# Performance work log

Hardware: AMD Instinct MI355X
Metric: run time of the kernel (lower is better)

## Reference

```python
import jax, jax.numpy as jnp
import numpy as np

N = 100000   # nodes
E = 1600000  # edges (avg degree 16)
R = 8        # relations
B = 4        # bases
IN = 128     # in_size
H = 128      # hidden_size
OUT = 64     # out_feats


def setup_inputs() -> dict:
    key = jax.random.key(0)
    k = jax.random.split(key, 14)
    sI = 1.0 / np.sqrt(IN)
    sH = 1.0 / np.sqrt(H)
    sB = 1.0 / np.sqrt(B)
    return {
        "feat": jax.random.normal(k[0], (N, IN), jnp.float32),
        "win": jax.random.normal(k[1], (IN, H), jnp.float32) * sI,
        "bin_": jnp.zeros((H,), jnp.float32),
        "basis0": jax.random.normal(k[2], (B, H, H), jnp.float32) * sH,
        "wcomp0": jax.random.normal(k[3], (R, B), jnp.float32) * sB,
        "loop0": jax.random.normal(k[4], (H, H), jnp.float32) * sH,
        "hbias0": jnp.zeros((H,), jnp.float32),
        "basis1": jax.random.normal(k[5], (B, H, H), jnp.float32) * sH,
        "wcomp1": jax.random.normal(k[6], (R, B), jnp.float32) * sB,
        "loop1": jax.random.normal(k[7], (H, H), jnp.float32) * sH,
        "hbias1": jnp.zeros((H,), jnp.float32),
        "wout": jax.random.normal(k[8], (H, OUT), jnp.float32) * sH,
        "bout": jnp.zeros((OUT,), jnp.float32),
        "src": jax.random.randint(k[9], (E,), 0, N),
        "dst": jax.random.randint(k[10], (E,), 0, N),
        "etypes": jax.random.randint(k[11], (E,), 0, R),
    }


def _rel_graph_conv(h, src, dst, etypes, basis, wcomp, loopw, hbias):
    """DGL RelGraphConv (basis regularizer, self_loop, bias, relu).

    out_i = relu( sum_r W_r * (sum_{e: dst_e=i, etype_e=r} h[src_e]) + h_i @ loopw + bias )
    Messages are linear, so we aggregate raw features by (dst, relation)
    composite key first, then apply the R per-relation matmuls once per node.
    """
    W = jnp.einsum('rb,bio->rio', wcomp, basis)          # [R, H, H] basis-composed weights
    seg = dst * R + etypes                               # composite (node, relation) key
    s = jax.ops.segment_sum(h[src], seg, num_segments=N * R)  # [N*R, H]
    s = s.reshape(N, R, -1)
    agg = jnp.einsum('nri,rio->no', s, W)                # [N, H]
    return jax.nn.relu(agg + hbias + h @ loopw)


def reference(feat, win, bin_, basis0, wcomp0, loop0, hbias0,
              basis1, wcomp1, loop1, hbias1, wout, bout, src, dst, etypes):
    h = jax.nn.relu(feat @ win + bin_)                   # input_layer
    h = _rel_graph_conv(h, src, dst, etypes, basis0, wcomp0, loop0, hbias0)
    h = _rel_graph_conv(h, src, dst, etypes, basis1, wcomp1, loop1, hbias1)
    return jax.nn.relu(h @ wout + bout)                  # out_layer
```

## Files before the change

kernel.cpp:

```cpp
#include <hip/hip_runtime.h>

#define NN   100000
#define EE   1600000
constexpr int RR = 8;
constexpr int BBASES = 4;
constexpr int SCAN_CHUNK = 1024;
constexpr int NBLK = (NN + SCAN_CHUNK - 1) / SCAN_CHUNK;
constexpr int NBUK = 98;
constexpr int EPB  = 4096;
constexpr int P1BLOCKS = (EE + EPB - 1) / EPB;

typedef __attribute__((ext_vector_type(8))) short short8;
typedef __attribute__((ext_vector_type(4))) float f32x4;

__device__ __forceinline__ unsigned pack2(float x, float y) {
    unsigned xu = __float_as_uint(x);
    unsigned yu = __float_as_uint(y);
    xu = (xu + 0x7fffu + ((xu >> 16) & 1u)) >> 16;
    yu = (yu + 0x7fffu + ((yu >> 16) & 1u)) & 0xffff0000u;
    return xu | yu;
}

__device__ __forceinline__ unsigned short bf16r(float x) {
    unsigned u = __float_as_uint(x);
    return (unsigned short)((u + 0x7fffu + ((u >> 16) & 1u)) >> 16);
}

__device__ __forceinline__ void async16(const void* g, void* l) {
    __builtin_amdgcn_global_load_lds(
        (const __attribute__((address_space(1))) void*)g,
        (__attribute__((address_space(3))) void*)l, 16, 0, 0);
}


__global__ __launch_bounds__(256) void count_kernel(const int* __restrict__ dst,
                                                    int* __restrict__ counts) {
    int e = blockIdx.x * 256 + threadIdx.x;
    if (e < EE) atomicAdd(&counts[dst[e]], 1);
}

__global__ __launch_bounds__(256) void scan1(const int* __restrict__ counts,
                                             int* __restrict__ offsets,
                                             int* __restrict__ totals) {
    __shared__ int lds[256];
    int b = blockIdx.x, tid = threadIdx.x;
    int base = b * SCAN_CHUNK + tid * 4;
    int v0 = (base + 0 < NN) ? counts[base + 0] : 0;
    int v1 = (base + 1 < NN) ? counts[base + 1] : 0;
    int v2 = (base + 2 < NN) ? counts[base + 2] : 0;
    int v3 = (base + 3 < NN) ? counts[base + 3] : 0;
    int s0 = v0, s1 = s0 + v1, s2 = s1 + v2, s3 = s2 + v3;
    lds[tid] = s3;
    __syncthreads();
    for (int d = 1; d < 256; d <<= 1) {
        int x = (tid >= d) ? lds[tid - d] : 0;
        __syncthreads();
        lds[tid] += x;
        __syncthreads();
    }
    int incl = lds[tid];
    int prefix = incl - s3;
    if (base + 0 < NN) offsets[base + 0] = prefix;
    if (base + 1 < NN) offsets[base + 1] = prefix + s0;
    if (base + 2 < NN) offsets[base + 2] = prefix + s1;
    if (base + 3 < NN) offsets[base + 3] = prefix + s2;
    if (tid == 255) totals[b] = lds[255];
}

__global__ __launch_bounds__(128) void scan2(int* __restrict__ totals,
                                             int* __restrict__ offsets,
                                             int* __restrict__ gcursor) {
    __shared__ int s[128];
    int tid = threadIdx.x;
    int v = (tid < NBLK) ? totals[tid] : 0;
    s[tid] = v;
    __syncthreads();
    for (int d = 1; d < 128; d <<= 1) {
        int x = (tid >= d) ? s[tid - d] : 0;
        __syncthreads();
        s[tid] += x;
        __syncthreads();
    }
    int excl = s[tid] - v;
    if (tid < NBLK) {
        totals[tid] = excl;
        gcursor[tid] = excl;
    }
    if (tid == NBLK - 1) offsets[NN] = excl + v;
}

__global__ __launch_bounds__(256) void scan3(int* __restrict__ offsets,
                                             const int* __restrict__ totals) {
    int i = blockIdx.x * 256 + threadIdx.x;
    if (i < NN) offsets[i] += totals[i >> 10];
}


__global__ __launch_bounds__(256) void bin_pass1(const int* __restrict__ src,
                                                 const int* __restrict__ dst,
                                                 const int* __restrict__ et,
                                                 int* __restrict__ gcursor,
                                                 unsigned* __restrict__ tmp) {
    __shared__ unsigned stage[EPB];
    __shared__ int hist[128];
    __shared__ int sc[128];
    __shared__ int lb[128];
    __shared__ int gb[128];
    int tid = threadIdx.x;
    long e0 = (long)blockIdx.x * EPB;
    if (tid < 128) hist[tid] = 0;
    __syncthreads();

    unsigned w[16];
    int bk[16], pos[16];
#pragma unroll
    for (int i = 0; i < 16; ++i) {
        long e = e0 + i * 256 + tid;
        bool valid = e < EE;
        int d = valid ? dst[e] : 0;
        int s = valid ? src[e] : 0;
        int r = valid ? et[e] : 0;
        bk[i] = d >> 10;
        w[i] = (unsigned)s | ((unsigned)r << 17) | ((unsigned)(d & 1023) << 20);
        pos[i] = valid ? atomicAdd(&hist[bk[i]], 1) : -1;
    }
    __syncthreads();
    if (tid < 128) sc[tid] = hist[tid];
    __syncthreads();
    for (int d = 1; d < 128; d <<= 1) {
        int v = 0;
        if (tid < 128 && tid >= d) v = sc[tid - d];
        __syncthreads();
        if (tid < 128) sc[tid] += v;
        __syncthreads();
    }
    if (tid < 128) lb[tid] = sc[tid] - hist[tid];
    if (tid < NBUK && hist[tid] > 0) gb[tid] = atomicAdd(&gcursor[tid], hist[tid]);
    __syncthreads();
    int total = sc[127];
#pragma unroll
    for (int i = 0; i < 16; ++i) {
        if (pos[i] >= 0) stage[lb[bk[i]] + pos[i]] = w[i];
    }
    __syncthreads();
    for (int s = tid; s < total; s += 256) {
        int lo = 0, hi = 127;
#pragma unroll
        for (int it = 0; it < 7; ++it) {
            int mid = (lo + hi + 1) >> 1;
            if (lb[mid] <= s) lo = mid; else hi = mid - 1;
        }
        tmp[gb[lo] + (s - lb[lo])] = stage[s];
    }
}

__global__ __launch_bounds__(1024) void bin_pass2(const unsigned* __restrict__ tmp,
                                                  const int* __restrict__ offsets,
                                                  int* __restrict__ packed) {
    __shared__ int cur[1024];
    __shared__ int offs[1025];
    int b = blockIdx.x, tid = threadIdx.x;
    int nb0 = b << 10;
    int nend = nb0 + 1024; if (nend > NN) nend = NN;
    int nloc = nend - nb0;
    cur[tid] = 0;
    for (int i = tid; i <= nloc; i += 1024) offs[i] = offsets[nb0 + i];
    __syncthreads();
    int beg = offs[0], end = offs[nloc];
    for (int e = beg + tid; e < end; e += 1024) {
        unsigned wv = tmp[e];
        int dl = (wv >> 20) & 1023;
        int p = offs[dl] + atomicAdd(&cur[dl], 1);
        packed[p] = (int)((wv & 0x1FFFFu) | (((wv >> 17) & 7u) << 20));
    }
}


__global__ __launch_bounds__(256) void convert_weights(const float* __restrict__ basis0,
                                                       const float* __restrict__ loop0,
                                                       const float* __restrict__ basis1,
                                                       const float* __restrict__ loop1,
                                                       const float* __restrict__ win,
                                                       const float* __restrict__ wout,
                                                       unsigned short* __restrict__ BT0,
                                                       unsigned short* __restrict__ BT1,
                                                       unsigned short* __restrict__ winT,
                                                       unsigned short* __restrict__ woutT) {
    int i = blockIdx.x * 256 + threadIdx.x;
    if (i < 81920) {
        int n = i / 640, k = i % 640;
        BT0[i] = bf16r(k < 512 ? basis0[(size_t)k * 128 + n] : loop0[(size_t)(k - 512) * 128 + n]);
    } else if (i < 163840) {
        int j = i - 81920;
        int n = j / 640, k = j % 640;
        BT1[j] = bf16r(k < 512 ? basis1[(size_t)k * 128 + n] : loop1[(size_t)(k - 512) * 128 + n]);
    } else if (i < 180224) {
        int j = i - 163840;
        int n = j >> 7, k = j & 127;
        winT[j] = bf16r(win[(size_t)k * 128 + n]);
    } else if (i < 188416) {
        int j = i - 180224;
        int n = j >> 7, k = j & 127;
        woutT[j] = bf16r(wout[(size_t)k * 64 + n]);
    }
}

template <int NC, bool F32OUT, bool AF32>
__global__ __launch_bounds__(256) void gemm128(const void* __restrict__ Aptr,
                                               const unsigned short* __restrict__ BT,
                                               const float* __restrict__ bias,
                                               void* __restrict__ outp, int M) {
    constexpr int NFRAG = NC / 32;
    constexpr int BQ = NC * 8 / 256;
    __shared__ __align__(16) char As[2][16384];
    __shared__ __align__(16) char Bs[2][NC * 128];
    int tid = threadIdx.x;
    int lane = tid & 63;
    int wave = tid >> 6;
    int wm = wave >> 1, wn = wave & 1;
    int m0 = blockIdx.x * 128;

    uint4 areg[4], breg[BQ];
    auto loadA = [&](int c) {
#pragma unroll
        for (int q = 0; q < 4; ++q) {
            int lin = q * 256 + tid;
            int row = lin >> 3, slot = lin & 7;
            int gr = m0 + row;
            gr = (gr < M) ? gr : (M - 1);
            if (AF32) {
                const float* fp = (const float*)Aptr + (size_t)gr * 128 + c * 64 + slot * 8;
                float4 v0 = *(const float4*)fp;
                float4 v1 = *(const float4*)(fp + 4);
                areg[q].x = pack2(v0.x, v0.y);
                areg[q].y = pack2(v0.z, v0.w);
                areg[q].z = pack2(v1.x, v1.y);
                areg[q].w = pack2(v1.z, v1.w);
            } else {
                areg[q] = *(const uint4*)((const char*)Aptr + (size_t)gr * 256 + c * 128 + slot * 16);
            }
        }
    };
    auto loadB = [&](int c) {
#pragma unroll
        for (int q = 0; q < BQ; ++q) {
            int lin = q * 256 + tid;
            int n = lin >> 3, slot = lin & 7;
            breg[q] = *(const uint4*)((const char*)BT + (size_t)n * 256 + c * 128 + slot * 16);
        }
    };

    f32x4 acc[4][NFRAG];
#pragma unroll
    for (int m = 0; m < 4; ++m)
#pragma unroll
        for (int n = 0; n < NFRAG; ++n) acc[m][n] = (f32x4)0.f;

    loadA(0); loadB(0);
    int swz = (lane & 7) << 4;

    for (int c = 0; c < 2; ++c) {
        int buf = c & 1;
#pragma unroll
        for (int q = 0; q < 4; ++q) {
            int lin = q * 256 + tid;
            int row = lin >> 3, slot = lin & 7;
            *(uint4*)(As[buf] + row * 128 + ((slot * 16) ^ ((row & 7) << 4))) = areg[q];
        }
#pragma unroll
        for (int q = 0; q < BQ; ++q) {
            int lin = q * 256 + tid;
            int row = lin >> 3, slot = lin & 7;
            *(uint4*)(Bs[buf] + row * 128 + ((slot * 16) ^ ((row & 7) << 4))) = breg[q];
        }
        __syncthreads();
        if (c < 1) { loadA(1); loadB(1); }
#pragma unroll
        for (int ks = 0; ks < 2; ++ks) {
            short8 a[4], b[NFRAG];
            int kb = ks * 64 + (lane >> 4) * 16;
#pragma unroll
            for (int m = 0; m < 4; ++m) {
                int row = wm * 64 + m * 16 + (lane & 15);
                a[m] = *(const short8*)(As[buf] + row * 128 + (kb ^ swz));
            }
#pragma unroll
            for (int n = 0; n < NFRAG; ++n) {
                int col = wn * (NC / 2) + n * 16 + (lane & 15);
                b[n] = *(const short8*)(Bs[buf] + col * 128 + (kb ^ swz));
            }
#pragma unroll
            for (int m = 0; m < 4; ++m)
#pragma unroll
                for (int n = 0; n < NFRAG; ++n)
                    acc[m][n] = __builtin_amdgcn_mfma_f32_16x16x32_bf16(a[m], b[n], acc[m][n], 0, 0, 0);
        }
        __syncthreads();
    }

    int colbase = wn * (NC / 2) + (lane & 15);
    float bias_v[NFRAG];
#pragma unroll
    for (int n = 0; n < NFRAG; ++n) bias_v[n] = bias[colbase + n * 16];
#pragma unroll
    for (int m = 0; m < 4; ++m) {
        int rl0 = m0 + wm * 64 + m * 16 + ((lane >> 4) << 2);
#pragma unroll
        for (int n = 0; n < NFRAG; ++n) {
            int col = colbase + n * 16;
#pragma unroll
            for (int q = 0; q < 4; ++q) {
                float v = fmaxf(acc[m][n][q] + bias_v[n], 0.f);
                int row = rl0 + q;
                if (F32OUT) {
                    if (row < M) ((float*)outp)[(size_t)row * NC + col] = v;
                } else {
                    float vo = __shfl_xor(v, 1);
                    if (((lane & 1) == 0) && row < M)
                        ((unsigned*)outp)[(size_t)row * (NC / 2) + (col >> 1)] = pack2(v, vo);
                }
            }
        }
    }
}


__global__ __launch_bounds__(256) void agg_kernel(const unsigned* __restrict__ hin,
                                                  const int* __restrict__ offsets,
                                                  const int* __restrict__ packed,
                                                  const float* __restrict__ wcomp,
                                                  unsigned* __restrict__ tbuf,
                                                  int chunk_start, int chunk_len) {
    __shared__ float wc[32];
    int tid = threadIdx.x;
    if (tid < 32) wc[tid] = wcomp[tid];
    __syncthreads();
    int nl = blockIdx.x * 4 + (tid >> 6);
    int lane = tid & 63;
    if (nl >= chunk_len) return;
    int n = chunk_start + nl;
    int beg = offsets[n], end = offsets[n + 1];
    float a0x = 0.f, a0y = 0.f, a1x = 0.f, a1y = 0.f;
    float a2x = 0.f, a2y = 0.f, a3x = 0.f, a3y = 0.f;
    auto edge = [&](unsigned u, unsigned hv) {
        int r = (int)(u >> 20);
        float hx = __uint_as_float(hv << 16);
        float hy = __uint_as_float(hv & 0xffff0000u);
        float w0 = wc[r * 4 + 0], w1 = wc[r * 4 + 1];
        float w2 = wc[r * 4 + 2], w3 = wc[r * 4 + 3];
        a0x = fmaf(w0, hx, a0x); a0y = fmaf(w0, hy, a0y);
        a1x = fmaf(w1, hx, a1x); a1y = fmaf(w1, hy, a1y);
        a2x = fmaf(w2, hx, a2x); a2y = fmaf(w2, hy, a2y);
        a3x = fmaf(w3, hx, a3x); a3y = fmaf(w3, hy, a3y);
    };
    int e = beg;
    int ehead = (beg + 3) & ~3;
    if (ehead > end) ehead = end;
    for (; e < ehead; ++e) {
        unsigned u = (unsigned)packed[e];
        unsigned hv = hin[(size_t)(u & 0xFFFFFu) * 64 + lane];
        edge(u, hv);
    }
    for (; e + 8 <= end; e += 8) {
        uint4 p0 = *(const uint4*)(packed + e);
        uint4 p1 = *(const uint4*)(packed + e + 4);
        unsigned h0 = hin[(size_t)(p0.x & 0xFFFFFu) * 64 + lane];
        unsigned h1 = hin[(size_t)(p0.y & 0xFFFFFu) * 64 + lane];
        unsigned h2 = hin[(size_t)(p0.z & 0xFFFFFu) * 64 + lane];
        unsigned h3 = hin[(size_t)(p0.w & 0xFFFFFu) * 64 + lane];
        unsigned h4 = hin[(size_t)(p1.x & 0xFFFFFu) * 64 + lane];
        unsigned h5 = hin[(size_t)(p1.y & 0xFFFFFu) * 64 + lane];
        unsigned h6 = hin[(size_t)(p1.z & 0xFFFFFu) * 64 + lane];
        unsigned h7 = hin[(size_t)(p1.w & 0xFFFFFu) * 64 + lane];
        edge(p0.x, h0); edge(p0.y, h1); edge(p0.z, h2); edge(p0.w, h3);
        edge(p1.x, h4); edge(p1.y, h5); edge(p1.z, h6); edge(p1.w, h7);
    }
    for (; e + 4 <= end; e += 4) {
        uint4 p0 = *(const uint4*)(packed + e);
        unsigned h0 = hin[(size_t)(p0.x & 0xFFFFFu) * 64 + lane];
        unsigned h1 = hin[(size_t)(p0.y & 0xFFFFFu) * 64 + lane];
        unsigned h2 = hin[(size_t)(p0.z & 0xFFFFFu) * 64 + lane];
        unsigned h3 = hin[(size_t)(p0.w & 0xFFFFFu) * 64 + lane];
        edge(p0.x, h0); edge(p0.y, h1); edge(p0.z, h2); edge(p0.w, h3);
    }
    for (; e < end; ++e) {
        unsigned u = (unsigned)packed[e];
        unsigned hv = hin[(size_t)(u & 0xFFFFFu) * 64 + lane];
        edge(u, hv);
    }
    size_t tb = (size_t)nl * 256 + lane;
    __builtin_nontemporal_store(pack2(a0x, a0y), &tbuf[tb + 0]);
    __builtin_nontemporal_store(pack2(a1x, a1y), &tbuf[tb + 64]);
    __builtin_nontemporal_store(pack2(a2x, a2y), &tbuf[tb + 128]);
    __builtin_nontemporal_store(pack2(a3x, a3y), &tbuf[tb + 192]);
}


template <bool FUSE_OUT>
__global__ __launch_bounds__(256) void conv_gemm(const unsigned* __restrict__ tbuf,
                                                 const unsigned* __restrict__ hin,
                                                 const unsigned short* __restrict__ BT,
                                                 const float* __restrict__ hbias,
                                                 unsigned* __restrict__ hout,
                                                 const unsigned short* __restrict__ WoutT,
                                                 const float* __restrict__ bout,
                                                 float* __restrict__ outp,
                                                 int chunk_start, int chunk_len) {
    __shared__ __align__(16) char As[2][16384];
    __shared__ __align__(16) char Bs[2][16384];
    __shared__ __align__(16) char Ws[16384];
    int tid = threadIdx.x;
    int lane = tid & 63;
    int wave = tid >> 6;
    int wm = wave >> 1, wn = wave & 1;
    int m0 = blockIdx.x * 128;

    auto stage = [&](int c, int buf) {
#pragma unroll
        for (int q = 0; q < 4; ++q) {
            int row = q * 32 + wave * 8 + (lane >> 3);
            int s_src = (lane & 7) ^ (lane >> 3);
            int lr = m0 + row;
            lr = (lr < chunk_len) ? lr : (chunk_len - 1);
            const char* ga = (c < 8)
                ? (const char*)(tbuf + (size_t)lr * 256) + c * 128 + s_src * 16
                : (const char*)(hin + (size_t)(chunk_start + lr) * 64) + (c - 8) * 128 + s_src * 16;
            async16(ga, &As[buf][q * 4096 + wave * 1024]);
            const char* gb = (const char*)BT + (size_t)row * 1280 + c * 128 + s_src * 16;
            async16(gb, &Bs[buf][q * 4096 + wave * 1024]);
        }
    };

    f32x4 acc[4][4];
#pragma unroll
    for (int m = 0; m < 4; ++m)
#pragma unroll
        for (int n = 0; n < 4; ++n) acc[m][n] = (f32x4)0.f;

    stage(0, 0);
    if (FUSE_OUT) {
#pragma unroll
        for (int q = 0; q < 4; ++q) {
            int row = q * 16 + wave * 4 + (lane >> 4);
            int s_src = (lane & 15) ^ (row & 7);
            async16((const char*)WoutT + (size_t)row * 256 + s_src * 16,
                    &Ws[q * 4096 + wave * 1024]);
        }
    }
    __syncthreads();
    int swz = (lane & 7) << 4;

    for (int c = 0; c < 10; ++c) {
        int buf = c & 1;
        if (c < 9) stage(c + 1, buf ^ 1);
#pragma unroll
        for (int ks = 0; ks < 2; ++ks) {
            short8 a[4], b[4];
            int kb = ks * 64 + (lane >> 4) * 16;
#pragma unroll
            for (int m = 0; m < 4; ++m) {
                int row = wm * 64 + m * 16 + (lane & 15);
                a[m] = *(const short8*)(As[buf] + row * 128 + (kb ^ swz));
            }
#pragma unroll
            for (int n = 0; n < 4; ++n) {
                int col = wn * 64 + n * 16 + (lane & 15);
                b[n] = *(const short8*)(Bs[buf] + col * 128 + (kb ^ swz));
            }
#pragma unroll
            for (int m = 0; m < 4; ++m)
#pragma unroll
                for (int n = 0; n < 4; ++n)
                    acc[m][n] = __builtin_amdgcn_mfma_f32_16x16x32_bf16(a[m], b[n], acc[m][n], 0, 0, 0);
        }
        __syncthreads();
    }

    unsigned* olds = (unsigned*)&As[0][0];
    int colbase = wn * 64 + (lane & 15);
    float bias_v[4];
#pragma unroll
    for (int n = 0; n < 4; ++n) bias_v[n] = hbias[colbase + n * 16];

    if (!FUSE_OUT) {
#pragma unroll
        for (int m = 0; m < 4; ++m) {
            int rbase = wm * 64 + m * 16 + ((lane >> 4) << 2);
#pragma unroll
            for (int n = 0; n < 4; ++n) {
#pragma unroll
                for (int q = 0; q < 4; ++q) {
                    float v = fmaxf(acc[m][n][q] + bias_v[n], 0.f);
                    float vo = __shfl_xor(v, 1);
                    if ((lane & 1) == 0) {
                        olds[(rbase + q) * 64 + wn * 32 + n * 8 + ((lane & 15) >> 1)] = pack2(v, vo);
                    }
                }
            }
        }
        __syncthreads();
#pragma unroll
        for (int i = 0; i < 8; ++i) {
            int j = i * 256 + tid;
            int row = j >> 4, s = j & 15;
            int gr = m0 + row;
            if (gr < chunk_len) {
                ((uint4*)(hout + (size_t)(chunk_start + gr) * 64))[s] = ((const uint4*)olds)[j];
            }
        }
    } else {
#pragma unroll
        for (int m = 0; m < 4; ++m) {
            int rbase = wm * 64 + m * 16 + ((lane >> 4) << 2);
#pragma unroll
            for (int n = 0; n < 4; ++n) {
#pragma unroll
                for (int q = 0; q < 4; ++q) {
                    float v = fmaxf(acc[m][n][q] + bias_v[n], 0.f);
                    float vo = __shfl_xor(v, 1);
                    if ((lane & 1) == 0) {
                        int row = rbase + q;
                        int d = wn * 32 + n * 8 + ((lane & 15) >> 1);
                        olds[row * 64 + (d ^ ((row & 7) << 2))] = pack2(v, vo);
                    }
                }
            }
        }
        __syncthreads();
        f32x4 acc2[4][2];
#pragma unroll
        for (int m = 0; m < 4; ++m)
#pragma unroll
            for (int n = 0; n < 2; ++n) acc2[m][n] = (f32x4)0.f;
#pragma unroll
        for (int ks = 0; ks < 4; ++ks) {
            int kb = ks * 64 + (lane >> 4) * 16;
            short8 a2[4], b2[2];
#pragma unroll
            for (int m = 0; m < 4; ++m) {
                int row = wm * 64 + m * 16 + (lane & 15);
                a2[m] = *(const short8*)((const char*)olds + row * 256 + (kb ^ ((row & 7) << 4)));
            }
#pragma unroll
            for (int n = 0; n < 2; ++n) {
                int col = wn * 32 + n * 16 + (lane & 15);
                b2[n] = *(const short8*)(Ws + col * 256 + (kb ^ ((col & 7) << 4)));
            }
#pragma unroll
            for (int m = 0; m < 4; ++m)
#pragma unroll
                for (int n = 0; n < 2; ++n)
                    acc2[m][n] = __builtin_amdgcn_mfma_f32_16x16x32_bf16(a2[m], b2[n], acc2[m][n], 0, 0, 0);
        }
        int colb = wn * 32 + (lane & 15);
        float bv2[2];
#pragma unroll
        for (int n = 0; n < 2; ++n) bv2[n] = bout[colb + n * 16];
#pragma unroll
        for (int m = 0; m < 4; ++m) {
            int rl0 = wm * 64 + m * 16 + ((lane >> 4) << 2);
#pragma unroll
            for (int n = 0; n < 2; ++n) {
#pragma unroll
                for (int q = 0; q < 4; ++q) {
                    int row = rl0 + q;
                    if (m0 + row < chunk_len) {
                        float v = fmaxf(acc2[m][n][q] + bv2[n], 0.f);
                        outp[(size_t)(chunk_start + m0 + row) * 64 + colb + n * 16] = v;
                    }
                }
            }
        }
    }
}


static inline size_t align256(size_t x) { return (x + 255) & ~(size_t)255; }

extern "C" void kernel_launch(void* const* d_in, const int* in_sizes, int n_in,
                              void* d_out, int out_size, void* d_ws, size_t ws_size,
                              hipStream_t stream) {
    const float* feat   = (const float*)d_in[0];
    const float* win    = (const float*)d_in[1];
    const float* bin_   = (const float*)d_in[2];
    const float* basis0 = (const float*)d_in[3];
    const float* wcomp0 = (const float*)d_in[4];
    const float* loop0  = (const float*)d_in[5];
    const float* hbias0 = (const float*)d_in[6];
    const float* basis1 = (const float*)d_in[7];
    const float* wcomp1 = (const float*)d_in[8];
    const float* loop1  = (const float*)d_in[9];
    const float* hbias1 = (const float*)d_in[10];
    const float* wout   = (const float*)d_in[11];
    const float* bout   = (const float*)d_in[12];
    const int*   src    = (const int*)d_in[13];
    const int*   dst    = (const int*)d_in[14];
    const int*   etyp   = (const int*)d_in[15];
    float* outp = (float*)d_out;

    size_t off = 0;
    char* wsb = (char*)d_ws;
    auto walloc = [&](size_t bytes) { void* p = wsb + off; off += align256(bytes); return p; };
    unsigned* hA  = (unsigned*)walloc((size_t)NN * 64 * 4);
    unsigned* hB  = (unsigned*)walloc((size_t)NN * 64 * 4);
    int* offsets  = (int*)walloc((size_t)(NN + 1) * 4);
    int* counts   = (int*)walloc((size_t)NN * 4);
    int* totals   = (int*)walloc((size_t)NBLK * 4);
    int* gcursor  = (int*)walloc((size_t)NBUK * 4);
    int* packed   = (int*)walloc((size_t)EE * 4);
    unsigned* tmp = (unsigned*)walloc((size_t)EE * 4);
    unsigned short* BT0 = (unsigned short*)walloc((size_t)128 * 640 * 2);
    unsigned short* BT1 = (unsigned short*)walloc((size_t)128 * 640 * 2);
    unsigned short* winT = (unsigned short*)walloc((size_t)128 * 128 * 2);
    unsigned short* woutT = (unsigned short*)walloc((size_t)64 * 128 * 2);
    size_t fixed = off;

    int nchunk = 1;
    while (nchunk < 32) {
        size_t rows = (size_t)(NN + nchunk - 1) / nchunk;
        if (fixed + rows * 1024 <= ws_size) break;
        nchunk *= 2;
    }
    int chunk_rows = (NN + nchunk - 1) / nchunk;
    unsigned* tbuf = (unsigned*)(wsb + fixed);

    hipMemsetAsync(counts, 0, (size_t)NN * 4, stream);
    count_kernel<<<(EE + 255) / 256, 256, 0, stream>>>(dst, counts);
    scan1<<<NBLK, 256, 0, stream>>>(counts, offsets, totals);
    scan2<<<1, 128, 0, stream>>>(totals, offsets, gcursor);
    scan3<<<(NN + 255) / 256, 256, 0, stream>>>(offsets, totals);
    bin_pass1<<<P1BLOCKS, 256, 0, stream>>>(src, dst, etyp, gcursor, tmp);
    bin_pass2<<<NBUK, 1024, 0, stream>>>(tmp, offsets, packed);

    convert_weights<<<(188416 + 255) / 256, 256, 0, stream>>>(
        basis0, loop0, basis1, loop1, win, wout, BT0, BT1, winT, woutT);

    int gblocks = (NN + 127) / 128;
    gemm128<128, false, true><<<gblocks, 256, 0, stream>>>(feat, winT, bin_, hA, NN);

    for (int s = 0; s < NN; s += chunk_rows) {
        int len = (NN - s < chunk_rows) ? (NN - s) : chunk_rows;
        agg_kernel<<<(len + 3) / 4, 256, 0, stream>>>(hA, offsets, packed, wcomp0, tbuf, s, len);
        conv_gemm<false><<<(len + 127) / 128, 256, 0, stream>>>(
            tbuf, hA, BT0, hbias0, hB, nullptr, nullptr, nullptr, s, len);
    }
    for (int s = 0; s < NN; s += chunk_rows) {
        int len = (NN - s < chunk_rows) ? (NN - s) : chunk_rows;
        agg_kernel<<<(len + 3) / 4, 256, 0, stream>>>(hB, offsets, packed, wcomp1, tbuf, s, len);
        conv_gemm<true><<<(len + 127) / 128, 256, 0, stream>>>(
            tbuf, hB, BT1, hbias1, nullptr, woutT, bout, outp, s, len);
    }
}
```

Measured before the change: 417.5 us.

## Sort edges by (dst, relation) and fold basis weights once per relation run

bin_pass2 now builds a per-block histogram over a combined dst-local and relation key, scans it in shared memory, and scatters edges so each node's edges are grouped by relation. The aggregation kernel then sums raw features within a relation run and applies the four basis coefficients only when the relation changes. This swaps eight FMAs per edge for two adds, at the cost of a heavier binning pass with a block-wide scan and divergent fold branches.

```diff
diff --git a/kernel.cpp b/kernel.cpp
--- a/kernel.cpp
+++ b/kernel.cpp
@@ -157,20 +157,39 @@
 __global__ __launch_bounds__(1024) void bin_pass2(const unsigned* __restrict__ tmp,
                                                   const int* __restrict__ offsets,
                                                   int* __restrict__ packed) {
-    __shared__ int cur[1024];
-    __shared__ int offs[1025];
+    __shared__ int hist[8192];
+    __shared__ int ssum[1024];
     int b = blockIdx.x, tid = threadIdx.x;
     int nb0 = b << 10;
     int nend = nb0 + 1024; if (nend > NN) nend = NN;
-    int nloc = nend - nb0;
-    cur[tid] = 0;
-    for (int i = tid; i <= nloc; i += 1024) offs[i] = offsets[nb0 + i];
-    __syncthreads();
-    int beg = offs[0], end = offs[nloc];
+    int beg = offsets[nb0], end = offsets[nend];
+#pragma unroll
+    for (int i = 0; i < 8; ++i) hist[tid * 8 + i] = 0;
+    __syncthreads();
     for (int e = beg + tid; e < end; e += 1024) {
         unsigned wv = tmp[e];
-        int dl = (wv >> 20) & 1023;
-        int p = offs[dl] + atomicAdd(&cur[dl], 1);
+        atomicAdd(&hist[(wv >> 17) & 8191], 1);
+    }
+    __syncthreads();
+    int loc[8];
+    int run = 0;
+#pragma unroll
+    for (int i = 0; i < 8; ++i) { loc[i] = run; run += hist[tid * 8 + i]; }
+    ssum[tid] = run;
+    __syncthreads();
+    for (int d = 1; d < 1024; d <<= 1) {
+        int x = (tid >= d) ? ssum[tid - d] : 0;
+        __syncthreads();
+        ssum[tid] += x;
+        __syncthreads();
+    }
+    int base = (tid > 0) ? ssum[tid - 1] : 0;
+#pragma unroll
+    for (int i = 0; i < 8; ++i) hist[tid * 8 + i] = base + loc[i];
+    __syncthreads();
+    for (int e = beg + tid; e < end; e += 1024) {
+        unsigned wv = tmp[e];
+        int p = beg + atomicAdd(&hist[(wv >> 17) & 8191], 1);
         packed[p] = (int)((wv & 0x1FFFFu) | (((wv >> 17) & 7u) << 20));
     }
 }
@@ -340,26 +359,38 @@
     if (nl >= chunk_len) return;
     int n = chunk_start + nl;
     int beg = offsets[n], end = offsets[n + 1];
-    float a0x = 0.f, a0y = 0.f, a1x = 0.f, a1y = 0.f;
-    float a2x = 0.f, a2y = 0.f, a3x = 0.f, a3y = 0.f;
-    auto edge = [&](unsigned u, unsigned hv) {
+
+    float t0 = 0.f, t1 = 0.f, t2 = 0.f, t3 = 0.f;
+    float t4 = 0.f, t5 = 0.f, t6 = 0.f, t7 = 0.f;
+    float sx = 0.f, sy = 0.f;
+    int rcur = -1;
+
+    auto fold = [&]() {
+        float w0 = wc[rcur * 4 + 0], w1 = wc[rcur * 4 + 1];
+        float w2 = wc[rcur * 4 + 2], w3 = wc[rcur * 4 + 3];
+        t0 = fmaf(w0, sx, t0); t1 = fmaf(w0, sy, t1);
+        t2 = fmaf(w1, sx, t2); t3 = fmaf(w1, sy, t3);
+        t4 = fmaf(w2, sx, t4); t5 = fmaf(w2, sy, t5);
+        t6 = fmaf(w3, sx, t6); t7 = fmaf(w3, sy, t7);
+        sx = 0.f; sy = 0.f;
+    };
+    auto acc1 = [&](unsigned u, unsigned hv) {
         int r = (int)(u >> 20);
-        float hx = __uint_as_float(hv << 16);
-        float hy = __uint_as_float(hv & 0xffff0000u);
-        float w0 = wc[r * 4 + 0], w1 = wc[r * 4 + 1];
-        float w2 = wc[r * 4 + 2], w3 = wc[r * 4 + 3];
-        a0x = fmaf(w0, hx, a0x); a0y = fmaf(w0, hy, a0y);
-        a1x = fmaf(w1, hx, a1x); a1y = fmaf(w1, hy, a1y);
-        a2x = fmaf(w2, hx, a2x); a2y = fmaf(w2, hy, a2y);
-        a3x = fmaf(w3, hx, a3x); a3y = fmaf(w3, hy, a3y);
+        if (r != rcur) {
+            if (rcur >= 0) fold();
+            rcur = r;
+        }
+        sx += __uint_as_float(hv << 16);
+        sy += __uint_as_float(hv & 0xffff0000u);
     };
+
     int e = beg;
     int ehead = (beg + 3) & ~3;
     if (ehead > end) ehead = end;
     for (; e < ehead; ++e) {
         unsigned u = (unsigned)packed[e];
         unsigned hv = hin[(size_t)(u & 0xFFFFFu) * 64 + lane];
-        edge(u, hv);
+        acc1(u, hv);
     }
     for (; e + 8 <= end; e += 8) {
         uint4 p0 = *(const uint4*)(packed + e);
@@ -372,8 +403,8 @@
         unsigned h5 = hin[(size_t)(p1.y & 0xFFFFFu) * 64 + lane];
         unsigned h6 = hin[(size_t)(p1.z & 0xFFFFFu) * 64 + lane];
         unsigned h7 = hin[(size_t)(p1.w & 0xFFFFFu) * 64 + lane];
-        edge(p0.x, h0); edge(p0.y, h1); edge(p0.z, h2); edge(p0.w, h3);
-        edge(p1.x, h4); edge(p1.y, h5); edge(p1.z, h6); edge(p1.w, h7);
+        acc1(p0.x, h0); acc1(p0.y, h1); acc1(p0.z, h2); acc1(p0.w, h3);
+        acc1(p1.x, h4); acc1(p1.y, h5); acc1(p1.z, h6); acc1(p1.w, h7);
     }
     for (; e + 4 <= end; e += 4) {
         uint4 p0 = *(const uint4*)(packed + e);
@@ -381,18 +412,20 @@
         unsigned h1 = hin[(size_t)(p0.y & 0xFFFFFu) * 64 + lane];
         unsigned h2 = hin[(size_t)(p0.z & 0xFFFFFu) * 64 + lane];
         unsigned h3 = hin[(size_t)(p0.w & 0xFFFFFu) * 64 + lane];
-        edge(p0.x, h0); edge(p0.y, h1); edge(p0.z, h2); edge(p0.w, h3);
+        acc1(p0.x, h0); acc1(p0.y, h1); acc1(p0.z, h2); acc1(p0.w, h3);
     }
     for (; e < end; ++e) {
         unsigned u = (unsigned)packed[e];
         unsigned hv = hin[(size_t)(u & 0xFFFFFu) * 64 + lane];
-        edge(u, hv);
-    }
+        acc1(u, hv);
+    }
+    if (rcur >= 0) fold();
+
     size_t tb = (size_t)nl * 256 + lane;
-    __builtin_nontemporal_store(pack2(a0x, a0y), &tbuf[tb + 0]);
-    __builtin_nontemporal_store(pack2(a1x, a1y), &tbuf[tb + 64]);
-    __builtin_nontemporal_store(pack2(a2x, a2y), &tbuf[tb + 128]);
-    __builtin_nontemporal_store(pack2(a3x, a3y), &tbuf[tb + 192]);
+    __builtin_nontemporal_store(pack2(t0, t1), &tbuf[tb + 0]);
+    __builtin_nontemporal_store(pack2(t2, t3), &tbuf[tb + 64]);
+    __builtin_nontemporal_store(pack2(t4, t5), &tbuf[tb + 128]);
+    __builtin_nontemporal_store(pack2(t6, t7), &tbuf[tb + 192]);
 }
 
 
```

Measured after the change: 424.7 us. No clear change (+1.7%).
